# Kernel optimization log

Hardware: AMD Instinct MI355X
Metric: run time of the kernel (lower is better)

Reference implementation:

```python
import jax, jax.numpy as jnp
import numpy as np

N = 50000        # number of nodes
E = 1600000      # number of (directed) edges, ~degree 32
D = 128          # latent_dim
L = 2            # num_layers
NEG_SLOPE = 0.01 # torch F.leaky_relu default


def setup_inputs() -> dict:
    key = jax.random.key(0)
    k1, k2, k3, k4 = jax.random.split(key, 4)
    h = jax.random.normal(k1, (N, D), dtype=jnp.float32)
    src = jax.random.randint(k2, (E,), 0, N, dtype=jnp.int32)
    dst = jax.random.randint(k3, (E,), 0, N, dtype=jnp.int32)
    # attn_fc per layer: Linear(2*D, 1, bias=False) -> weight vector of length 2*D
    att_w = jax.random.normal(k4, (L, 2 * D), dtype=jnp.float32) * 0.1
    return {"h": h, "src": src, "dst": dst, "att_w": att_w}


def _segment_softmax(e, seg, n):
    # numerically-stable softmax over edges grouped by destination node
    m = jax.ops.segment_max(e, seg, num_segments=n)      # [N]
    ex = jnp.exp(e - m[seg])                             # [E]
    s = jax.ops.segment_sum(ex, seg, num_segments=n)     # [N]
    return ex / s[seg]


def reference(h, src, dst, att_w):
    n, d = h.shape
    for l in range(att_w.shape[0]):
        w_src = att_w[l, :d]   # weight applied to edges.src['h']
        w_dst = att_w[l, d:]   # weight applied to edges.dst['h']
        # a = attn_fc(concat(h_src, h_dst)) = h_src @ w_src + h_dst @ w_dst
        a = h[src] @ w_src + h[dst] @ w_dst               # [E]
        e = jnp.where(a > 0, a, NEG_SLOPE * a)            # leaky_relu
        alpha = _segment_softmax(e, dst, n)               # edge_softmax by dst
        # update_all: m = h_src * e ; h_dst = sum(m)
        h = jax.ops.segment_sum(h[src] * alpha[:, None], dst, num_segments=n)
    return h
```

## Files before the change

### kernel.cpp

```cpp
#include <hip/hip_runtime.h>
#include <hip/hip_fp16.h>
#include <math.h>

#define NEG_SLOPE 0.01f
#define BKT_BITS 7
#define BKT_MASK 127
#define SBLOCKS  256
#define STPB     512
#define MAXNB    512
#define SEG_BITS 13
#define SEG_CAP  (1 << SEG_BITS)


__global__ void build_st_kernel(const int* __restrict__ src, const int* __restrict__ dst,
                                int* __restrict__ g_total, unsigned* __restrict__ pairs,
                                int E, int NB, int nq, int qchunk,
                                const float* __restrict__ h, const float* __restrict__ att_w_l,
                                float* __restrict__ s, float* __restrict__ t,
                                __half* __restrict__ h16, int N) {
    extern __shared__ int lm[];
    if (blockIdx.x < SBLOCKS) {
        int* lh  = lm;
        int* lbb = lm + NB;
        for (int k = threadIdx.x; k < NB; k += blockDim.x) lh[k] = 0;
        __syncthreads();
        int b = blockIdx.x;
        int qbeg = b * qchunk, qend = min(nq, qbeg + qchunk);
        for (int q = qbeg + (int)threadIdx.x; q < qend; q += blockDim.x) {
            int e = q << 2;
            if (e + 3 < E) {
                int4 d4 = *(const int4*)(dst + e);
                atomicAdd(&lh[d4.x >> BKT_BITS], 1);
                atomicAdd(&lh[d4.y >> BKT_BITS], 1);
                atomicAdd(&lh[d4.z >> BKT_BITS], 1);
                atomicAdd(&lh[d4.w >> BKT_BITS], 1);
            } else {
                for (int j = e; j < E; ++j) atomicAdd(&lh[dst[j] >> BKT_BITS], 1);
            }
        }
        __syncthreads();
        for (int k = threadIdx.x; k < NB; k += blockDim.x) {
            lbb[k] = atomicAdd(&g_total[k], lh[k]);
            lh[k]  = 0;
        }
        __syncthreads();
        for (int q = qbeg + (int)threadIdx.x; q < qend; q += blockDim.x) {
            int e = q << 2;
            if (e + 3 < E) {
                int4 d4 = *(const int4*)(dst + e);
                int4 s4 = *(const int4*)(src + e);
                int k0 = d4.x >> BKT_BITS;
                int p0 = lbb[k0] + atomicAdd(&lh[k0], 1);
                if (p0 < SEG_CAP)
                    pairs[(k0 << SEG_BITS) + p0] = ((unsigned)s4.x << BKT_BITS) | (unsigned)(d4.x & BKT_MASK);
                int k1 = d4.y >> BKT_BITS;
                int p1 = lbb[k1] + atomicAdd(&lh[k1], 1);
                if (p1 < SEG_CAP)
                    pairs[(k1 << SEG_BITS) + p1] = ((unsigned)s4.y << BKT_BITS) | (unsigned)(d4.y & BKT_MASK);
                int k2 = d4.z >> BKT_BITS;
                int p2 = lbb[k2] + atomicAdd(&lh[k2], 1);
                if (p2 < SEG_CAP)
                    pairs[(k2 << SEG_BITS) + p2] = ((unsigned)s4.z << BKT_BITS) | (unsigned)(d4.z & BKT_MASK);
                int k3 = d4.w >> BKT_BITS;
                int p3 = lbb[k3] + atomicAdd(&lh[k3], 1);
                if (p3 < SEG_CAP)
                    pairs[(k3 << SEG_BITS) + p3] = ((unsigned)s4.w << BKT_BITS) | (unsigned)(d4.w & BKT_MASK);
            } else {
                for (int j = e; j < E; ++j) {
                    int d = dst[j];
                    int k = d >> BKT_BITS;
                    int pos = lbb[k] + atomicAdd(&lh[k], 1);
                    if (pos < SEG_CAP)
                        pairs[(k << SEG_BITS) + pos] = ((unsigned)src[j] << BKT_BITS) | (unsigned)(d & BKT_MASK);
                }
            }
        }
    } else {
        int sb  = blockIdx.x - SBLOCKS;
        int gid = sb * (int)blockDim.x + threadIdx.x;
        int wid = gid >> 6;
        int lane = threadIdx.x & 63;
        int half = lane >> 5;
        int hl   = lane & 31;
        int v    = wid * 2 + half;
        if (v >= N) return;
        float4 hv = ((const float4*)(h + (size_t)v * 128))[hl];
        __half2 p01 = __floats2half2_rn(hv.x, hv.y);
        __half2 p23 = __floats2half2_rn(hv.z, hv.w);
        float2 packed;
        packed.x = *(const float*)&p01;
        packed.y = *(const float*)&p23;
        ((float2*)(h16 + (size_t)v * 128))[hl] = packed;
        float4 ws = ((const float4*)att_w_l)[hl];
        float4 wd = ((const float4*)(att_w_l + 128))[hl];
        float ps = hv.x * ws.x + hv.y * ws.y + hv.z * ws.z + hv.w * ws.w;
        float pt = hv.x * wd.x + hv.y * wd.y + hv.z * wd.z + hv.w * wd.w;
        for (int off = 16; off > 0; off >>= 1) {
            ps += __shfl_down(ps, off);
            pt += __shfl_down(pt, off);
        }
        if (hl == 0) { s[v] = ps; t[v] = pt; }
    }
}

__global__ void csr_build_kernel(const unsigned* __restrict__ pairs,
                                 const int* __restrict__ g_total,
                                 int* __restrict__ row_beg, int* __restrict__ row_end,
                                 int* __restrict__ csr_src, int N, int NB) {
    __shared__ int ldeg[128];
    __shared__ int lscan[128];
    __shared__ int lpos[128];
    int k = blockIdx.x;
    int sbase = k << SEG_BITS;
    int cnt = min(g_total[k], SEG_CAP);
    if (threadIdx.x < 128) ldeg[threadIdx.x] = 0;
    __syncthreads();
    for (int i = threadIdx.x; i < cnt; i += blockDim.x)
        atomicAdd(&ldeg[pairs[sbase + i] & BKT_MASK], 1);
    __syncthreads();
    int x = (threadIdx.x < 128) ? ldeg[threadIdx.x] : 0;
    if (threadIdx.x < 128) lscan[threadIdx.x] = x;
    __syncthreads();
    for (int off = 1; off < 128; off <<= 1) {
        int y = 0;
        if (threadIdx.x < 128 && threadIdx.x >= (unsigned)off) y = lscan[threadIdx.x - off];
        __syncthreads();
        if (threadIdx.x < 128) lscan[threadIdx.x] += y;
        __syncthreads();
    }
    if (threadIdx.x < 128) {
        int excl = lscan[threadIdx.x] - x;
        int node = (k << BKT_BITS) + threadIdx.x;
        if (node < N) {
            row_beg[node] = sbase + excl;
            row_end[node] = sbase + excl + x;
        }
        lpos[threadIdx.x] = excl;
    }
    __syncthreads();
    for (int i = threadIdx.x; i < cnt; i += blockDim.x) {
        unsigned p = pairs[sbase + i];
        int pos = atomicAdd(&lpos[p & BKT_MASK], 1);
        csr_src[sbase + pos] = (int)(p >> BKT_BITS);
    }
}


__device__ __forceinline__ void gath8(const __half* __restrict__ hin, int u, float w,
                                      int qlane, float acc[8]) {
    float4 r = ((const float4*)(hin + ((size_t)(unsigned)u << 7)))[qlane];
    const __half2* hp = (const __half2*)&r;
    #pragma unroll
    for (int d = 0; d < 4; ++d) {
        acc[2 * d]     = fmaf(__low2float(hp[d]),  w, acc[2 * d]);
        acc[2 * d + 1] = fmaf(__high2float(hp[d]), w, acc[2 * d + 1]);
    }
}

template<bool LAST>
__global__ __launch_bounds__(256, 8)
void agg_kernel(const __half* __restrict__ hin, const float* __restrict__ s,
                const float* __restrict__ t, const int* __restrict__ row_beg,
                const int* __restrict__ row_end, const int* __restrict__ csr_src,
                __half* __restrict__ hout16, float* __restrict__ outf,
                const float* __restrict__ att_w_next,
                float* __restrict__ s2, float* __restrict__ t2, int n) {
    int gid   = blockIdx.x * blockDim.x + threadIdx.x;
    int v     = gid >> 6;
    int lane  = threadIdx.x & 63;
    if (v >= n) return;
    int quad  = lane >> 4;
    int qlane = lane & 15;

    int beg = row_beg[v];
    int end = row_end[v];
    float tv = t[v];

    float acc[8] = {0.f, 0.f, 0.f, 0.f, 0.f, 0.f, 0.f, 0.f};
    float lsum_l = 0.f;

    for (int base = beg; base < end; base += 64) {
        int cnt = end - base;
        if (cnt > 64) cnt = 64;
        int idx = base + min(lane, cnt - 1);
        int u   = csr_src[idx];
        float a = s[u] + tv;
        float e = (a > 0.f) ? a : NEG_SLOPE * a;
        float wl = (lane < cnt) ? __expf(e) : 0.f;
        lsum_l += wl;
        int steps = (cnt + 3) >> 2;
        int k = 0;
        for (; k + 3 < steps; k += 4) {
            int sl0 = (k << 2) + quad;
            int   u0 = __shfl(u, sl0);       float w0 = __shfl(wl, sl0);
            int   u1 = __shfl(u, sl0 + 4);   float w1 = __shfl(wl, sl0 + 4);
            int   u2 = __shfl(u, sl0 + 8);   float w2 = __shfl(wl, sl0 + 8);
            int   u3 = __shfl(u, sl0 + 12);  float w3 = __shfl(wl, sl0 + 12);
            gath8(hin, u0, w0, qlane, acc);
            gath8(hin, u1, w1, qlane, acc);
            gath8(hin, u2, w2, qlane, acc);
            gath8(hin, u3, w3, qlane, acc);
        }
        for (; k < steps; ++k) {
            int sl = (k << 2) + quad;
            int   u0 = __shfl(u, sl);
            float w0 = __shfl(wl, sl);
            gath8(hin, u0, w0, qlane, acc);
        }
    }
    #pragma unroll
    for (int j = 0; j < 8; ++j) {
        acc[j] += __shfl_xor(acc[j], 16);
        acc[j] += __shfl_xor(acc[j], 32);
    }
    float lsum = lsum_l;
    for (int off = 32; off > 0; off >>= 1) lsum += __shfl_xor(lsum, off);
    float inv_l = (lsum > 0.f) ? (1.0f / lsum) : 0.f;
    #pragma unroll
    for (int j = 0; j < 8; ++j) acc[j] *= inv_l;

    if (LAST) {
        if (quad == 0) {
            float4* op = (float4*)(outf + (size_t)v * 128);
            op[2 * qlane]     = make_float4(acc[0], acc[1], acc[2], acc[3]);
            op[2 * qlane + 1] = make_float4(acc[4], acc[5], acc[6], acc[7]);
        }
    } else {
        if (quad == 0) {
            __half2 p0 = __floats2half2_rn(acc[0], acc[1]);
            __half2 p1 = __floats2half2_rn(acc[2], acc[3]);
            __half2 p2 = __floats2half2_rn(acc[4], acc[5]);
            __half2 p3 = __floats2half2_rn(acc[6], acc[7]);
            int4 pk;
            pk.x = *(const int*)&p0; pk.y = *(const int*)&p1;
            pk.z = *(const int*)&p2; pk.w = *(const int*)&p3;
            ((int4*)(hout16 + (size_t)v * 128))[qlane] = pk;
        }
        float4 ws0 = ((const float4*)att_w_next)[2 * qlane];
        float4 ws1 = ((const float4*)att_w_next)[2 * qlane + 1];
        float4 wd0 = ((const float4*)(att_w_next + 128))[2 * qlane];
        float4 wd1 = ((const float4*)(att_w_next + 128))[2 * qlane + 1];
        float ps = acc[0] * ws0.x + acc[1] * ws0.y + acc[2] * ws0.z + acc[3] * ws0.w
                 + acc[4] * ws1.x + acc[5] * ws1.y + acc[6] * ws1.z + acc[7] * ws1.w;
        float pt = acc[0] * wd0.x + acc[1] * wd0.y + acc[2] * wd0.z + acc[3] * wd0.w
                 + acc[4] * wd1.x + acc[5] * wd1.y + acc[6] * wd1.z + acc[7] * wd1.w;
        for (int off = 8; off > 0; off >>= 1) {
            ps += __shfl_down(ps, off);
            pt += __shfl_down(pt, off);
        }
        if (lane == 0) { s2[v] = ps; t2[v] = pt; }
    }
}


extern "C" void kernel_launch(void* const* d_in, const int* in_sizes, int n_in,
                              void* d_out, int out_size, void* d_ws, size_t ws_size,
                              hipStream_t stream) {
    const float* h0    = (const float*)d_in[0];
    const int*   src   = (const int*)d_in[1];
    const int*   dst   = (const int*)d_in[2];
    const float* att_w = (const float*)d_in[3];
    int N = in_sizes[0] / 128;
    int E = in_sizes[1];
    int L = in_sizes[3] / 256;
    float* out = (float*)d_out;

    int NB = (N + BKT_MASK) >> BKT_BITS;
    int nq = (E + 3) >> 2;
    int qchunk = (nq + SBLOCKS - 1) / SBLOCKS;

    char* ws = (char*)d_ws;
    size_t off = 0;
    auto alloc = [&](size_t bytes) -> void* {
        void* p = ws + off;
        off = (off + bytes + 511) & ~(size_t)511;
        return p;
    };
    int*      row_beg   = (int*)     alloc((size_t)N * 4);
    int*      row_end   = (int*)     alloc((size_t)N * 4);
    int*      csr_src   = (int*)     alloc((size_t)NB << SEG_BITS << 2);
    unsigned* pairs     = (unsigned*)alloc((size_t)NB << SEG_BITS << 2);
    float*    s1        = (float*)   alloc((size_t)N * 4);
    float*    t1        = (float*)   alloc((size_t)N * 4);
    float*    s2        = (float*)   alloc((size_t)N * 4);
    float*    t2        = (float*)   alloc((size_t)N * 4);
    __half*   hA        = (__half*)  alloc((size_t)N * 128 * 2);
    __half*   hB        = (__half*)  alloc((size_t)N * 128 * 2);
    int*      g_total   = (int*)     alloc((size_t)(NB + 1) * 4);

    hipMemsetAsync(g_total, 0, (size_t)NB * 4, stream);

    int st_blocks = ((N + 1) / 2 + 7) / 8;
    build_st_kernel<<<SBLOCKS + st_blocks, STPB, 2 * NB * 4, stream>>>(
        src, dst, g_total, pairs, E, NB, nq, qchunk, h0, att_w, s1, t1, hA, N);
    csr_build_kernel<<<NB, 512, 0, stream>>>(pairs, g_total, row_beg, row_end,
                                             csr_src, N, NB);

    const int tb = 256;
    int node_blocks = (N * 64 + tb - 1) / tb;

    __half* hin = hA;
    __half* hnx = hB;
    float *sc = s1, *tc = t1, *sn = s2, *tn = t2;
    for (int l = 0; l < L; ++l) {
        if (l == L - 1) {
            agg_kernel<true><<<node_blocks, tb, 0, stream>>>(
                hin, sc, tc, row_beg, row_end, csr_src,
                nullptr, out, nullptr, nullptr, nullptr, N);
        } else {
            agg_kernel<false><<<node_blocks, tb, 0, stream>>>(
                hin, sc, tc, row_beg, row_end, csr_src,
                hnx, nullptr, att_w + (size_t)(l + 1) * 256, sn, tn, N);
            __half* tmp = hin; hin = hnx; hnx = tmp;
            float* tf;
            tf = sc; sc = sn; sn = tf;
            tf = tc; tc = tn; tn = tf;
        }
    }
}
```

Baseline: 216.9 us.

## Stage edge tiles in LDS and shrink buckets for CSR build

The bucket-scatter kernel now loads each tile of src/dst into shared memory once and reuses it for both the histogram and scatter passes, instead of reading dst twice from global memory. Bucket size is halved (64 nodes per bucket, 4096-slot segments) with twice as many scatter blocks, and the CSR build kernel reads pairs as uint4 with 256 threads. The change trades extra shared memory (about 33 KB static per block, which lowers occupancy for the s/t blocks too) and more global atomics on g_total per tile for less global traffic and more parallelism. Smaller segments also raise the risk of overflowing SEG_CAP with uneven degree distributions.

```diff
diff --git a/kernel.cpp b/kernel.cpp
--- a/kernel.cpp
+++ b/kernel.cpp
@@ -3,13 +3,14 @@
 #include <math.h>
 
 #define NEG_SLOPE 0.01f
-#define BKT_BITS 7
-#define BKT_MASK 127
-#define SBLOCKS  256
+#define BKT_BITS 6
+#define BKT_MASK 63
+#define SBLOCKS  512
 #define STPB     512
-#define MAXNB    512
-#define SEG_BITS 13
+#define MAXNB    1024
+#define SEG_BITS 12
 #define SEG_CAP  (1 << SEG_BITS)
+#define MAXT     3200
 
 
 __global__ void build_st_kernel(const int* __restrict__ src, const int* __restrict__ dst,
@@ -18,68 +19,65 @@
                                 const float* __restrict__ h, const float* __restrict__ att_w_l,
                                 float* __restrict__ s, float* __restrict__ t,
                                 __half* __restrict__ h16, int N) {
-    extern __shared__ int lm[];
+    __shared__ int lh[MAXNB];
+    __shared__ int lbb[MAXNB];
+    __shared__ int lsrc[MAXT];
+    __shared__ int ldst[MAXT];
+    int tid = threadIdx.x;
     if (blockIdx.x < SBLOCKS) {
-        int* lh  = lm;
-        int* lbb = lm + NB;
-        for (int k = threadIdx.x; k < NB; k += blockDim.x) lh[k] = 0;
-        __syncthreads();
         int b = blockIdx.x;
         int qbeg = b * qchunk, qend = min(nq, qbeg + qchunk);
-        for (int q = qbeg + (int)threadIdx.x; q < qend; q += blockDim.x) {
-            int e = q << 2;
-            if (e + 3 < E) {
-                int4 d4 = *(const int4*)(dst + e);
-                atomicAdd(&lh[d4.x >> BKT_BITS], 1);
-                atomicAdd(&lh[d4.y >> BKT_BITS], 1);
-                atomicAdd(&lh[d4.z >> BKT_BITS], 1);
-                atomicAdd(&lh[d4.w >> BKT_BITS], 1);
-            } else {
-                for (int j = e; j < E; ++j) atomicAdd(&lh[dst[j] >> BKT_BITS], 1);
+        for (int t0 = qbeg; t0 < qend; t0 += MAXT / 4) {
+            int t1 = min(qend, t0 + MAXT / 4);
+            int nt = (t1 - t0) << 2;
+            for (int k = tid; k < NB; k += blockDim.x) lh[k] = 0;
+            __syncthreads();
+            for (int q = t0 + tid; q < t1; q += blockDim.x) {
+                int e  = q << 2;
+                int li = (q - t0) << 2;
+                if (e + 3 < E) {
+                    int4 d4 = *(const int4*)(dst + e);
+                    int4 s4 = *(const int4*)(src + e);
+                    lsrc[li] = s4.x; ldst[li] = d4.x; atomicAdd(&lh[d4.x >> BKT_BITS], 1);
+                    lsrc[li + 1] = s4.y; ldst[li + 1] = d4.y; atomicAdd(&lh[d4.y >> BKT_BITS], 1);
+                    lsrc[li + 2] = s4.z; ldst[li + 2] = d4.z; atomicAdd(&lh[d4.z >> BKT_BITS], 1);
+                    lsrc[li + 3] = s4.w; ldst[li + 3] = d4.w; atomicAdd(&lh[d4.w >> BKT_BITS], 1);
+                } else {
+                    for (int j = 0; j < 4; ++j) {
+                        int e2 = e + j, li2 = li + j;
+                        if (e2 < E) {
+                            int d = dst[e2];
+                            lsrc[li2] = src[e2]; ldst[li2] = d;
+                            atomicAdd(&lh[d >> BKT_BITS], 1);
+                        } else {
+                            ldst[li2] = -1;
+                        }
+                    }
+                }
             }
-        }
-        __syncthreads();
-        for (int k = threadIdx.x; k < NB; k += blockDim.x) {
-            lbb[k] = atomicAdd(&g_total[k], lh[k]);
-            lh[k]  = 0;
-        }
-        __syncthreads();
-        for (int q = qbeg + (int)threadIdx.x; q < qend; q += blockDim.x) {
-            int e = q << 2;
-            if (e + 3 < E) {
-                int4 d4 = *(const int4*)(dst + e);
-                int4 s4 = *(const int4*)(src + e);
-                int k0 = d4.x >> BKT_BITS;
-                int p0 = lbb[k0] + atomicAdd(&lh[k0], 1);
-                if (p0 < SEG_CAP)
-                    pairs[(k0 << SEG_BITS) + p0] = ((unsigned)s4.x << BKT_BITS) | (unsigned)(d4.x & BKT_MASK);
-                int k1 = d4.y >> BKT_BITS;
-                int p1 = lbb[k1] + atomicAdd(&lh[k1], 1);
-                if (p1 < SEG_CAP)
-                    pairs[(k1 << SEG_BITS) + p1] = ((unsigned)s4.y << BKT_BITS) | (unsigned)(d4.y & BKT_MASK);
-                int k2 = d4.z >> BKT_BITS;
-                int p2 = lbb[k2] + atomicAdd(&lh[k2], 1);
-                if (p2 < SEG_CAP)
-                    pairs[(k2 << SEG_BITS) + p2] = ((unsigned)s4.z << BKT_BITS) | (unsigned)(d4.z & BKT_MASK);
-                int k3 = d4.w >> BKT_BITS;
-                int p3 = lbb[k3] + atomicAdd(&lh[k3], 1);
-                if (p3 < SEG_CAP)
-                    pairs[(k3 << SEG_BITS) + p3] = ((unsigned)s4.w << BKT_BITS) | (unsigned)(d4.w & BKT_MASK);
-            } else {
-                for (int j = e; j < E; ++j) {
-                    int d = dst[j];
+            __syncthreads();
+            for (int k = tid; k < NB; k += blockDim.x) {
+                lbb[k] = atomicAdd(&g_total[k], lh[k]);
+                lh[k]  = 0;
+            }
+            __syncthreads();
+            for (int i = tid; i < nt; i += blockDim.x) {
+                int d = ldst[i];
+                if (d >= 0) {
                     int k = d >> BKT_BITS;
                     int pos = lbb[k] + atomicAdd(&lh[k], 1);
                     if (pos < SEG_CAP)
-                        pairs[(k << SEG_BITS) + pos] = ((unsigned)src[j] << BKT_BITS) | (unsigned)(d & BKT_MASK);
+                        pairs[(k << SEG_BITS) + pos] =
+                            ((unsigned)lsrc[i] << BKT_BITS) | (unsigned)(d & BKT_MASK);
                 }
             }
+            __syncthreads();
         }
     } else {
         int sb  = blockIdx.x - SBLOCKS;
-        int gid = sb * (int)blockDim.x + threadIdx.x;
+        int gid = sb * (int)blockDim.x + tid;
         int wid = gid >> 6;
-        int lane = threadIdx.x & 63;
+        int lane = tid & 63;
         int half = lane >> 5;
         int hl   = lane & 31;
         int v    = wid * 2 + half;
@@ -107,38 +105,54 @@
                                  const int* __restrict__ g_total,
                                  int* __restrict__ row_beg, int* __restrict__ row_end,
                                  int* __restrict__ csr_src, int N, int NB) {
-    __shared__ int ldeg[128];
-    __shared__ int lscan[128];
-    __shared__ int lpos[128];
+    __shared__ int ldeg[64];
+    __shared__ int lscan[64];
+    __shared__ int lpos[64];
+    int tid = threadIdx.x;
     int k = blockIdx.x;
     int sbase = k << SEG_BITS;
     int cnt = min(g_total[k], SEG_CAP);
-    if (threadIdx.x < 128) ldeg[threadIdx.x] = 0;
+    if (tid < 64) ldeg[tid] = 0;
     __syncthreads();
-    for (int i = threadIdx.x; i < cnt; i += blockDim.x)
+    int body = cnt & ~3;
+    for (int i = tid * 4; i < body; i += blockDim.x * 4) {
+        uint4 p4 = *(const uint4*)(pairs + sbase + i);
+        atomicAdd(&ldeg[p4.x & BKT_MASK], 1);
+        atomicAdd(&ldeg[p4.y & BKT_MASK], 1);
+        atomicAdd(&ldeg[p4.z & BKT_MASK], 1);
+        atomicAdd(&ldeg[p4.w & BKT_MASK], 1);
+    }
+    for (int i = body + tid; i < cnt; i += blockDim.x)
         atomicAdd(&ldeg[pairs[sbase + i] & BKT_MASK], 1);
     __syncthreads();
-    int x = (threadIdx.x < 128) ? ldeg[threadIdx.x] : 0;
-    if (threadIdx.x < 128) lscan[threadIdx.x] = x;
+    int x = (tid < 64) ? ldeg[tid] : 0;
+    if (tid < 64) lscan[tid] = x;
     __syncthreads();
-    for (int off = 1; off < 128; off <<= 1) {
+    for (int off = 1; off < 64; off <<= 1) {
         int y = 0;
-        if (threadIdx.x < 128 && threadIdx.x >= (unsigned)off) y = lscan[threadIdx.x - off];
+        if (tid < 64 && tid >= (unsigned)off) y = lscan[tid - off];
         __syncthreads();
-        if (threadIdx.x < 128) lscan[threadIdx.x] += y;
+        if (tid < 64) lscan[tid] += y;
         __syncthreads();
     }
-    if (threadIdx.x < 128) {
-        int excl = lscan[threadIdx.x] - x;
-        int node = (k << BKT_BITS) + threadIdx.x;
+    if (tid < 64) {
+        int excl = lscan[tid] - x;
+        int node = (k << BKT_BITS) + tid;
         if (node < N) {
             row_beg[node] = sbase + excl;
             row_end[node] = sbase + excl + x;
         }
-        lpos[threadIdx.x] = excl;
+        lpos[tid] = excl;
     }
     __syncthreads();
-    for (int i = threadIdx.x; i < cnt; i += blockDim.x) {
+    for (int i = tid * 4; i < body; i += blockDim.x * 4) {
+        uint4 p4 = *(const uint4*)(pairs + sbase + i);
+        int p0 = atomicAdd(&lpos[p4.x & BKT_MASK], 1); csr_src[sbase + p0] = (int)(p4.x >> BKT_BITS);
+        int p1 = atomicAdd(&lpos[p4.y & BKT_MASK], 1); csr_src[sbase + p1] = (int)(p4.y >> BKT_BITS);
+        int p2 = atomicAdd(&lpos[p4.z & BKT_MASK], 1); csr_src[sbase + p2] = (int)(p4.z >> BKT_BITS);
+        int p3 = atomicAdd(&lpos[p4.w & BKT_MASK], 1); csr_src[sbase + p3] = (int)(p4.w >> BKT_BITS);
+    }
+    for (int i = body + tid; i < cnt; i += blockDim.x) {
         unsigned p = pairs[sbase + i];
         int pos = atomicAdd(&lpos[p & BKT_MASK], 1);
         csr_src[sbase + pos] = (int)(p >> BKT_BITS);
@@ -291,9 +305,9 @@
     hipMemsetAsync(g_total, 0, (size_t)NB * 4, stream);
 
     int st_blocks = ((N + 1) / 2 + 7) / 8;
-    build_st_kernel<<<SBLOCKS + st_blocks, STPB, 2 * NB * 4, stream>>>(
+    build_st_kernel<<<SBLOCKS + st_blocks, STPB, 0, stream>>>(
         src, dst, g_total, pairs, E, NB, nq, qchunk, h0, att_w, s1, t1, hA, N);
-    csr_build_kernel<<<NB, 512, 0, stream>>>(pairs, g_total, row_beg, row_end,
+    csr_build_kernel<<<NB, 256, 0, stream>>>(pairs, g_total, row_beg, row_end,
                                              csr_src, N, NB);
 
     const int tb = 256;
```

New measurement: 217.4 us. About the same (+0.3%).
